# Optimization experiments

Hardware: AMD Instinct MI355X
Metric: run time of the kernel (lower is better)

Reference implementation:

```python
import jax, jax.numpy as jnp
import numpy as np

A = 128       # atom_fea_len
NBR = 41      # nbr_fea_len
H = 128       # h_fea_len_dist == h_fea_len_const
NCONV = 3
EPS = 1e-5    # BatchNorm eps


def leaky(x):
    return jnp.where(x >= 0, x, 0.01 * x)  # LeakyReLU(0.01)


def bn(x2d, g, b):
    # training-mode BatchNorm1d: batch statistics over dim 0 (biased variance)
    mu = x2d.mean(0)
    var = x2d.var(0)
    return g * (x2d - mu) * jax.lax.rsqrt(var + EPS) + b


def setup_inputs() -> dict:
    N, M = 20000, 12
    key = jax.random.key(0)
    ks = jax.random.split(key, 24)
    s = 0.02
    in2 = 2 * A + NBR  # 297
    d = {}
    d["atom_fea"] = jax.random.normal(ks[0], (N, 92), jnp.float32)
    d["nbr_fea"] = jax.random.uniform(ks[1], (N, M, NBR), dtype=jnp.float32)
    d["nbr_fea_offset"] = jax.random.normal(ks[2], (N, M, 3), jnp.float32)
    d["atom_pos"] = jax.random.normal(ks[3], (N, 3), jnp.float32) * 3.0
    d["cells"] = jnp.eye(3, dtype=jnp.float32) * 10.0 + 0.1 * jax.random.normal(ks[4], (3, 3), jnp.float32)
    d["nbr_fea_idx"] = jax.random.randint(ks[5], (N, M), 0, N)
    # embedding
    d["emb_W"] = s * jax.random.normal(ks[6], (A, 92), jnp.float32)
    d["emb_b"] = jnp.zeros((A,), jnp.float32)
    # conv layers (stacked)
    d["convs_W"] = s * jax.random.normal(ks[7], (NCONV, 2 * A, in2), jnp.float32)
    d["convs_b"] = jnp.zeros((NCONV, 2 * A), jnp.float32)
    d["convs_bn1_g"] = jnp.ones((NCONV, 2 * A), jnp.float32)
    d["convs_bn1_b"] = jnp.zeros((NCONV, 2 * A), jnp.float32)
    d["convs_bn2_g"] = jnp.ones((NCONV, A), jnp.float32)
    d["convs_bn2_b"] = jnp.zeros((NCONV, A), jnp.float32)
    # bond_distance head
    d["dist_W"] = s * jax.random.normal(ks[8], (H, in2), jnp.float32)
    d["dist_b"] = jnp.zeros((H,), jnp.float32)
    d["dist_bn_g"] = jnp.ones((H,), jnp.float32)
    d["dist_bn_b"] = jnp.zeros((H,), jnp.float32)
    d["dist2_W"] = s * jax.random.normal(ks[9], (1, H), jnp.float32)
    d["dist2_b"] = jnp.zeros((1,), jnp.float32)
    # bond_constant head
    d["const_W"] = s * jax.random.normal(ks[10], (H, in2), jnp.float32)
    d["const_b"] = jnp.zeros((H,), jnp.float32)
    d["const_bn_g"] = jnp.ones((H,), jnp.float32)
    d["const_bn_b"] = jnp.zeros((H,), jnp.float32)
    d["const2_W"] = s * jax.random.normal(ks[11], (1, H), jnp.float32)
    d["const2_b"] = jnp.zeros((1,), jnp.float32)
    return d


def _forward(atom_fea, nbr_fea, nbr_fea_offset, atom_pos, cells,
             emb_W, emb_b, convs_W, convs_b, convs_bn1_g, convs_bn1_b,
             convs_bn2_g, convs_bn2_b, dist_W, dist_b, dist_bn_g, dist_bn_b,
             dist2_W, dist2_b, const_W, const_b, const_bn_g, const_bn_b,
             const2_W, const2_b, nbr_fea_idx):
    N, M = nbr_fea_idx.shape
    af = atom_fea @ emb_W.T + emb_b  # (N, A) embedding

    # get_distance: PBC distance using fractional offsets and the cell matrix
    nbr_abs = atom_pos[nbr_fea_idx] + jnp.einsum('nmk,kd->nmd', nbr_fea_offset, cells)
    dvec = nbr_abs - atom_pos[:, None, :]
    distance = jnp.sqrt(jnp.sum(dvec * dvec, -1, keepdims=True) + 1e-12)  # (N, M, 1)

    # conv layers: gather -> concat -> linear -> bn -> gate -> sum -> bn -> residual
    for i in range(NCONV):
        total = jnp.concatenate([
            jnp.broadcast_to(af[:, None, :], (N, M, A)),
            af[nbr_fea_idx],
            nbr_fea], axis=2)                                   # (N, M, 2A+NBR)
        g = jnp.einsum('nmf,of->nmo', total, convs_W[i]) + convs_b[i]  # (N, M, 2A)
        g = bn(g.reshape(-1, 2 * A), convs_bn1_g[i], convs_bn1_b[i]).reshape(N, M, 2 * A)
        nbr_filter = jax.nn.sigmoid(g[..., :A])
        nbr_core = leaky(g[..., A:])
        summed = bn((nbr_filter * nbr_core).sum(1), convs_bn2_g[i], convs_bn2_b[i])
        af = leaky(af + summed)

    # bond features
    bond_fea = jnp.concatenate([
        jnp.broadcast_to(af[:, None, :], (N, M, A)),
        af[nbr_fea_idx],
        nbr_fea], axis=2)  # (N, M, 2A+NBR)

    # bond_distance head (LeakyReLU activations)
    bd = jnp.einsum('nmf,hf->nmh', bond_fea, dist_W) + dist_b
    bd = leaky(bn(bd.reshape(-1, H), dist_bn_g, dist_bn_b).reshape(N, M, H))
    bd = leaky(jnp.einsum('nmh,oh->nmo', bd, dist2_W) + dist2_b + distance)  # (N, M, 1)

    # bond_constant head (Softplus activations)
    bc = jnp.einsum('nmf,hf->nmh', bond_fea, const_W) + const_b
    bc = jax.nn.softplus(bn(bc.reshape(-1, H), const_bn_g, const_bn_b).reshape(N, M, H))
    bc = jax.nn.softplus(jnp.einsum('nmh,oh->nmo', bc, const2_W) + const2_b)  # (N, M, 1)

    return jnp.concatenate([bd, bc], axis=-1)  # (N, M, 2)


def reference(atom_fea, nbr_fea, nbr_fea_offset, atom_pos, cells,
              emb_W, emb_b, convs_W, convs_b, convs_bn1_g, convs_bn1_b,
              convs_bn2_g, convs_bn2_b, dist_W, dist_b, dist_bn_g, dist_bn_b,
              dist2_W, dist2_b, const_W, const_b, const_bn_g, const_bn_b,
              const2_W, const2_b, nbr_fea_idx):
    return _forward(atom_fea, nbr_fea, nbr_fea_offset, atom_pos, cells,
                    emb_W, emb_b, convs_W, convs_b, convs_bn1_g, convs_bn1_b,
                    convs_bn2_g, convs_bn2_b, dist_W, dist_b, dist_bn_g, dist_bn_b,
                    dist2_W, dist2_b, const_W, const_b, const_bn_g, const_bn_b,
                    const2_W, const2_b, nbr_fea_idx)
```

## Files before the change

kernel.cpp:

```cpp
#include <hip/hip_runtime.h>
#include <hip/hip_bf16.h>
#include <math.h>

typedef __hip_bfloat16 bf16;

#define AFEA 128
#define NBRF 41
#define IN2 297
#define KP 320
#define TSTR 328
#define TSTRE 104
#define ROWS 64
#define P1 64
#define P2 16
#define WBE_OFF (4 * KP * 256)
#define WBE_SZ (3 * 128 * 32)

typedef __attribute__((ext_vector_type(8))) short bf16x8;
typedef __attribute__((ext_vector_type(4))) float f32x4;

__device__ __forceinline__ unsigned short bfbits(float x) {
    bf16 h = __float2bfloat16(x);
    return *(unsigned short*)&h;
}
__device__ __forceinline__ unsigned int pack2(float x, float y) {
    return (unsigned int)bfbits(x) | ((unsigned int)bfbits(y) << 16);
}
__device__ __forceinline__ float blo(unsigned int u) { return __uint_as_float(u << 16); }
__device__ __forceinline__ float bhi(unsigned int u) { return __uint_as_float(u & 0xffff0000u); }
__device__ __forceinline__ float leakyf(float x) { return x >= 0.f ? x : 0.01f * x; }
__device__ __forceinline__ float sigmoid_fast(float x) {
    return __builtin_amdgcn_rcpf(1.f + __expf(-x));
}
__device__ __forceinline__ float softplus_fast(float x) {
    return fmaxf(x, 0.f) + __logf(1.f + __expf(-fabsf(x)));
}

__device__ __forceinline__ float gpair(unsigned int fu, unsigned int cu,
                                       float aF, float cF, float aC, float cC) {
    float r = sigmoid_fast(fmaf(aF, blo(fu), cF)) * leakyf(fmaf(aC, blo(cu), cC));
    r += sigmoid_fast(fmaf(aF, bhi(fu), cF)) * leakyf(fmaf(aC, bhi(cu), cC));
    return r;
}

__global__ void nbr16_kernel(const float* __restrict__ nbr, unsigned short* __restrict__ nbr16,
                             int NM)
{
    int i = blockIdx.x * blockDim.x + threadIdx.x;
    if (i >= NM * 64) return;
    int k = i & 63, e = i >> 6;
    nbr16[i] = (k < NBRF) ? bfbits(nbr[(size_t)e * NBRF + k]) : 0;
}

__global__ __launch_bounds__(256) void embed_mfma_kernel(
    const float* __restrict__ xf, const unsigned short* __restrict__ WbE,
    const float* __restrict__ b, float* __restrict__ af,
    unsigned short* __restrict__ af16, int N)
{
    __shared__ __align__(16) unsigned short ls[64 * TSTRE];
    int t = threadIdx.x;
    const int e0 = blockIdx.x * 64;
    const int l = t & 63, w = t >> 6, m16 = l & 15, q = l >> 4;

    {
        int r = t >> 2, p = t & 3;
        int n = e0 + r;
        const float* src = xf + (size_t)n * 92;
        unsigned short* dst = ls + r * TSTRE;
        #pragma unroll
        for (int u = 0; u < 6; u++) {
            int k0 = p * 24 + u * 4;
            if (k0 < 92) {
                float4 v = (n < N) ? *(const float4*)(src + k0)
                                   : make_float4(0.f, 0.f, 0.f, 0.f);
                ushort4 h;
                h.x = bfbits(v.x); h.y = bfbits(v.y);
                h.z = bfbits(v.z); h.w = bfbits(v.w);
                *(ushort4*)(dst + k0) = h;
            }
        }
        if (p == 3) {
            ushort4 z = {0, 0, 0, 0};
            *(ushort4*)(dst + 92) = z;
        }
    }

    const unsigned short* bbase = WbE + (size_t)(w * 32 + m16) * 32 + q * 8;
    __syncthreads();

    f32x4 acc[4][2];
    #pragma unroll
    for (int rt = 0; rt < 4; rt++)
        #pragma unroll
        for (int ct = 0; ct < 2; ct++) acc[rt][ct] = (f32x4)0.f;

    const unsigned short* abase = ls + m16 * TSTRE + q * 8;

    #pragma unroll
    for (int kc = 0; kc < 3; kc++) {
        bf16x8 a[4], bfr[2];
        #pragma unroll
        for (int ct = 0; ct < 2; ct++)
            bfr[ct] = *(const bf16x8*)(bbase + kc * 4096 + ct * 512);
        #pragma unroll
        for (int rt = 0; rt < 4; rt++)
            a[rt] = *(const bf16x8*)(abase + rt * 16 * TSTRE + kc * 32);
        #pragma unroll
        for (int rt = 0; rt < 4; rt++)
            #pragma unroll
            for (int ct = 0; ct < 2; ct++)
                acc[rt][ct] = __builtin_amdgcn_mfma_f32_16x16x32_bf16(
                    a[rt], bfr[ct], acc[rt][ct], 0, 0, 0);
    }

    #pragma unroll
    for (int ct = 0; ct < 2; ct++) {
        int col = w * 32 + ct * 16 + m16;
        float bias = b[col];
        #pragma unroll
        for (int rt = 0; rt < 4; rt++) {
            #pragma unroll
            for (int j = 0; j < 4; j++) {
                int n = e0 + rt * 16 + q * 4 + j;
                if (n < N) {
                    float v = acc[rt][ct][j] + bias;
                    af[(size_t)n * AFEA + col] = v;
                    af16[(size_t)n * AFEA + col] = bfbits(v);
                }
            }
        }
    }
}

__global__ void prep_all_kernel(const float* __restrict__ convs_W,
                                const float* __restrict__ dist_W,
                                const float* __restrict__ const_W,
                                const float* __restrict__ emb_W,
                                unsigned short* __restrict__ Wb4,
                                float* __restrict__ zbuf, int nz)
{
    int i = blockIdx.x * blockDim.x + threadIdx.x;
    if (i < nz) zbuf[i] = 0.f;
    if (i >= WBE_OFF + WBE_SZ) return;
    if (i >= WBE_OFF) {
        int r2 = i - WBE_OFF;
        int t32 = r2 & 31, c = (r2 >> 5) & 127, kc = r2 >> 12;
        int k = kc * 32 + t32;
        Wb4[i] = bfbits((k < 92) ? emb_W[(size_t)c * 92 + k] : 0.f);
        return;
    }
    int s = i / (KP * 256);
    int r = i - s * (KP * 256);
    int t32 = r & 31;
    int c = (r >> 5) & 255;
    int kc = r >> 13;
    int k = kc * 32 + t32;
    float v = 0.f;
    if (k < IN2) {
        if (s < 3) v = convs_W[((size_t)s * 256 + c) * IN2 + k];
        else       v = (c < 128) ? dist_W[(size_t)c * IN2 + k]
                                 : const_W[(size_t)(c - 128) * IN2 + k];
    }
    Wb4[i] = bfbits(v);
}

__device__ __forceinline__ void gemm_core(
    const unsigned short* __restrict__ af16, const unsigned short* __restrict__ nbr16,
    const int* __restrict__ idx, const unsigned short* __restrict__ Wb,
    unsigned short* a_tile, int e0, int M, int t, f32x4 (&acc)[4][4])
{
    const int l = t & 63, w = t >> 6;
    const int m16 = l & 15, q = l >> 4;
    const unsigned short* bbase = Wb + (size_t)(w * 64 + m16) * 32 + q * 8;

    {
        int row = t >> 2, p = t & 3;
        int e = e0 + row;
        int n = e / M;
        int j = idx[e];
        const uint4* srcn = (const uint4*)(af16 + (size_t)n * AFEA);
        const uint4* srcj = (const uint4*)(af16 + (size_t)j * AFEA);
        const uint4* srcb = (const uint4*)(nbr16 + (size_t)e * 64);
        uint4* dst = (uint4*)(a_tile + row * TSTR);
        #pragma unroll
        for (int u = 0; u < 4; u++) dst[p + 4 * u] = srcn[p + 4 * u];
        #pragma unroll
        for (int u = 0; u < 4; u++) dst[16 + p + 4 * u] = srcj[p + 4 * u];
        #pragma unroll
        for (int u = 0; u < 2; u++) dst[32 + p + 4 * u] = srcb[p + 4 * u];
    }

    bf16x8 bcur[4], bnxt[4];
    #pragma unroll
    for (int ct = 0; ct < 4; ct++)
        bcur[ct] = *(const bf16x8*)(bbase + ct * 512);
    #pragma unroll
    for (int ct = 0; ct < 4; ct++)
        bnxt[ct] = *(const bf16x8*)(bbase + 8192 + ct * 512);

    __syncthreads();

    #pragma unroll
    for (int rt = 0; rt < 4; rt++)
        #pragma unroll
        for (int ct = 0; ct < 4; ct++) acc[rt][ct] = (f32x4)0.f;

    const unsigned short* abase = a_tile + m16 * TSTR + q * 8;

    #pragma unroll
    for (int kc = 0; kc < KP / 32; kc++) {
        bf16x8 a[4], b2[4];
        if (kc < KP / 32 - 2) {
            #pragma unroll
            for (int ct = 0; ct < 4; ct++)
                b2[ct] = *(const bf16x8*)(bbase + (kc + 2) * 8192 + ct * 512);
        }
        #pragma unroll
        for (int rt = 0; rt < 4; rt++)
            a[rt] = *(const bf16x8*)(abase + rt * 16 * TSTR + kc * 32);
        #pragma unroll
        for (int rt = 0; rt < 4; rt++)
            #pragma unroll
            for (int ct = 0; ct < 4; ct++)
                acc[rt][ct] = __builtin_amdgcn_mfma_f32_16x16x32_bf16(
                    a[rt], bcur[ct], acc[rt][ct], 0, 0, 0);
        if (kc < KP / 32 - 1) {
            #pragma unroll
            for (int ct = 0; ct < 4; ct++) bcur[ct] = bnxt[ct];
        }
        if (kc < KP / 32 - 2) {
            #pragma unroll
            for (int ct = 0; ct < 4; ct++) bnxt[ct] = b2[ct];
        }
    }
}

__global__ __launch_bounds__(256, 3) void gemm_mfma_kernel(
    const unsigned short* __restrict__ af16, const unsigned short* __restrict__ nbr16,
    const int* __restrict__ idx, const unsigned short* __restrict__ Wb,
    const float* __restrict__ bias_a, const float* __restrict__ bias_b,
    unsigned short* __restrict__ g_t, float* __restrict__ part1,
    float* __restrict__ part2, int NM, int M)
{
    __shared__ __align__(16) unsigned short a_tile[ROWS * TSTR];
    int t = threadIdx.x;
    const int e0 = blockIdx.x * ROWS;

    if (blockIdx.x < 16) part2[blockIdx.x * 256 + t] = 0.f;

    f32x4 acc[4][4];
    gemm_core(af16, nbr16, idx, Wb, a_tile, e0, M, t, acc);

    const int l = t & 63, w = t >> 6, m16 = l & 15, q = l >> 4;
    float* pp = part1 + (size_t)(blockIdx.x & (P1 - 1)) * 512;
    #pragma unroll
    for (int ct = 0; ct < 4; ct++) {
        int col = w * 64 + ct * 16 + m16;
        float bias = (col < 128) ? bias_a[col] : bias_b[col - 128];
        float ps = 0.f, pq = 0.f;
        #pragma unroll
        for (int rt = 0; rt < 4; rt++) {
            float v0 = acc[rt][ct][0] + bias;
            float v1 = acc[rt][ct][1] + bias;
            float v2 = acc[rt][ct][2] + bias;
            float v3 = acc[rt][ct][3] + bias;
            ps += (v0 + v1) + (v2 + v3);
            pq += (v0 * v0 + v1 * v1) + (v2 * v2 + v3 * v3);
            uint2 pk;
            pk.x = pack2(v0, v1);
            pk.y = pack2(v2, v3);
            *(uint2*)(g_t + (size_t)col * NM + e0 + rt * 16 + q * 4) = pk;
        }
        ps += __shfl_xor(ps, 16); ps += __shfl_xor(ps, 32);
        pq += __shfl_xor(pq, 16); pq += __shfl_xor(pq, 32);
        if (q == 0) {
            atomicAdd(&pp[col], ps);
            atomicAdd(&pp[256 + col], pq);
        }
    }
}

__global__ __launch_bounds__(256) void gate_kernel(
    const unsigned short* __restrict__ gt, const float* __restrict__ part1,
    const float* __restrict__ gamma, const float* __restrict__ beta,
    float* __restrict__ summed, float* __restrict__ part2,
    float cnt1, int N, int NM)
{
    __shared__ float affA[32], affC[32];
    __shared__ float ls[128 * 17];
    int t = threadIdx.x, w = t >> 6, l = t & 63;
    int ab = blockIdx.x >> 3, pg = blockIdx.x & 7;

    if (t < 32) {
        int ch = (t < 16) ? (pg * 16 + t) : (128 + pg * 16 + (t - 16));
        float s = 0.f, qq = 0.f;
        #pragma unroll 8
        for (int p = 0; p < P1; p++) {
            s += part1[(size_t)p * 512 + ch];
            qq += part1[(size_t)p * 512 + 256 + ch];
        }
        float mean = s / cnt1;
        float var = fmaxf(qq / cnt1 - mean * mean, 0.f);
        float a = gamma[ch] * rsqrtf(var + 1e-5f);
        affA[t] = a;
        affC[t] = beta[ch] - mean * a;
    }
    __syncthreads();

    int n0 = ab * 128 + 2 * l;
    bool a0 = n0 < N, a1 = (n0 + 1) < N;
    float* pp = part2 + (size_t)(blockIdx.x & (P2 - 1)) * 256;

    #pragma unroll
    for (int pi = 0; pi < 4; pi++) {
        int plocal = w * 4 + pi;
        int chf = pg * 16 + plocal;
        float aF = affA[plocal],      cF = affC[plocal];
        float aC = affA[16 + plocal], cC = affC[16 + plocal];
        float s0 = 0.f, s1 = 0.f;
        if (a0) {
            const uint4* F = (const uint4*)(gt + (size_t)chf * NM + (size_t)n0 * 12);
            const uint4* C = (const uint4*)(gt + (size_t)(chf + 128) * NM + (size_t)n0 * 12);
            uint4 f0 = F[0], f1 = F[1], f2 = F[2];
            uint4 c0 = C[0], c1 = C[1], c2 = C[2];
            s0 = gpair(f0.x, c0.x, aF, cF, aC, cC) + gpair(f0.y, c0.y, aF, cF, aC, cC)
               + gpair(f0.z, c0.z, aF, cF, aC, cC) + gpair(f0.w, c0.w, aF, cF, aC, cC)
               + gpair(f1.x, c1.x, aF, cF, aC, cC) + gpair(f1.y, c1.y, aF, cF, aC, cC);
            s1 = gpair(f1.z, c1.z, aF, cF, aC, cC) + gpair(f1.w, c1.w, aF, cF, aC, cC)
               + gpair(f2.x, c2.x, aF, cF, aC, cC) + gpair(f2.y, c2.y, aF, cF, aC, cC)
               + gpair(f2.z, c2.z, aF, cF, aC, cC) + gpair(f2.w, c2.w, aF, cF, aC, cC);
            if (!a1) s1 = 0.f;
            ls[(2 * l) * 17 + plocal] = s0;
            if (a1) ls[(2 * l + 1) * 17 + plocal] = s1;
        }
        float sr = s0 + s1;
        float qr = s0 * s0 + s1 * s1;
        #pragma unroll
        for (int sft = 32; sft > 0; sft >>= 1) {
            sr += __shfl_xor(sr, sft);
            qr += __shfl_xor(qr, sft);
        }
        if (l == 0) {
            atomicAdd(&pp[chf], sr);
            atomicAdd(&pp[128 + chf], qr);
        }
    }
    __syncthreads();

    for (int i = t; i < 128 * 16; i += 256) {
        int a = i >> 4, c = i & 15;
        int n = ab * 128 + a;
        if (n < N) summed[(size_t)n * AFEA + pg * 16 + c] = ls[a * 17 + c];
    }
}

__global__ __launch_bounds__(256) void afup_kernel(
    float* __restrict__ af, unsigned short* __restrict__ af16,
    const float* __restrict__ summed, const float* __restrict__ part2,
    const float* __restrict__ gamma2, const float* __restrict__ beta2,
    float* __restrict__ part1, float cnt2, int total)
{
    __shared__ float a2s[128], c2s[128];
    int t = threadIdx.x;
    if (blockIdx.x < 128) part1[blockIdx.x * 256 + t] = 0.f;
    if (t < 128) {
        float s = 0.f, qq = 0.f;
        #pragma unroll
        for (int p = 0; p < P2; p++) {
            s += part2[(size_t)p * 256 + t];
            qq += part2[(size_t)p * 256 + 128 + t];
        }
        float mean = s / cnt2;
        float var = fmaxf(qq / cnt2 - mean * mean, 0.f);
        float a = gamma2[t] * rsqrtf(var + 1e-5f);
        a2s[t] = a;
        c2s[t] = beta2[t] - mean * a;
    }
    __syncthreads();
    int o = t & 127;
    float a2 = a2s[o], c2 = c2s[o];
    int base = blockIdx.x * 2048 + t;
    #pragma unroll
    for (int k = 0; k < 8; k++) {
        int i = base + k * 256;
        if (i < total) {
            float v = af[i] + a2 * summed[i] + c2;
            v = (v >= 0.f) ? v : 0.01f * v;
            af[i] = v;
            af16[i] = bfbits(v);
        }
    }
}

__global__ __launch_bounds__(256) void head_kernel(
    const unsigned short* __restrict__ gt, const float* __restrict__ part1,
    const float* __restrict__ dbg, const float* __restrict__ cbg,
    const float* __restrict__ dbb, const float* __restrict__ cbb,
    const float* __restrict__ w2d, const float* __restrict__ b2d,
    const float* __restrict__ w2c, const float* __restrict__ b2c,
    const float* __restrict__ pos, const float* __restrict__ off,
    const float* __restrict__ cells, const int* __restrict__ idx,
    float* __restrict__ out, float cnt1, int NM, int M)
{
    __shared__ float a_s[256], c_s[256], w_s[256];
    int t = threadIdx.x;
    {
        float s = 0.f, qq = 0.f;
        #pragma unroll 8
        for (int p = 0; p < P1; p++) {
            s += part1[(size_t)p * 512 + t];
            qq += part1[(size_t)p * 512 + 256 + t];
        }
        float mean = s / cnt1;
        float var = fmaxf(qq / cnt1 - mean * mean, 0.f);
        float g  = (t < 128) ? dbg[t] : cbg[t - 128];
        float be = (t < 128) ? dbb[t] : cbb[t - 128];
        float a = g * rsqrtf(var + 1e-5f);
        a_s[t] = a;
        c_s[t] = be - mean * a;
        w_s[t] = (t < 128) ? w2d[t] : w2c[t - 128];
    }
    __syncthreads();

    int e = blockIdx.x * 512 + t * 2;
    if (e >= NM) return;
    float sd0 = 0.f, sd1 = 0.f, sc0 = 0.f, sc1 = 0.f;
    #pragma unroll 4
    for (int ch = 0; ch < 128; ch++) {
        unsigned int u = *(const unsigned int*)(gt + (size_t)ch * NM + e);
        float a = a_s[ch], c = c_s[ch], wv = w_s[ch];
        sd0 += leakyf(fmaf(a, blo(u), c)) * wv;
        sd1 += leakyf(fmaf(a, bhi(u), c)) * wv;
    }
    #pragma unroll 4
    for (int ch = 128; ch < 256; ch++) {
        unsigned int u = *(const unsigned int*)(gt + (size_t)ch * NM + e);
        float a = a_s[ch], c = c_s[ch], wv = w_s[ch];
        sc0 += softplus_fast(fmaf(a, blo(u), c)) * wv;
        sc1 += softplus_fast(fmaf(a, bhi(u), c)) * wv;
    }
    float dist[2];
    #pragma unroll
    for (int h = 0; h < 2; h++) {
        int eb = e + h;
        int n = eb / M;
        int j = idx[eb];
        float o0 = off[(size_t)eb * 3 + 0];
        float o1 = off[(size_t)eb * 3 + 1];
        float o2 = off[(size_t)eb * 3 + 2];
        float d0 = o0 * cells[0] + o1 * cells[3] + o2 * cells[6] + pos[(size_t)j * 3 + 0] - pos[(size_t)n * 3 + 0];
        float d1 = o0 * cells[1] + o1 * cells[4] + o2 * cells[7] + pos[(size_t)j * 3 + 1] - pos[(size_t)n * 3 + 1];
        float d2 = o0 * cells[2] + o1 * cells[5] + o2 * cells[8] + pos[(size_t)j * 3 + 2] - pos[(size_t)n * 3 + 2];
        dist[h] = sqrtf(d0 * d0 + d1 * d1 + d2 * d2 + 1e-12f);
    }
    float bd = b2d[0], bc = b2c[0];
    float4 o4;
    o4.x = leakyf(sd0 + bd + dist[0]);
    o4.y = softplus_fast(sc0 + bc);
    o4.z = leakyf(sd1 + bd + dist[1]);
    o4.w = softplus_fast(sc1 + bc);
    *(float4*)(out + (size_t)e * 2) = o4;
}

extern "C" void kernel_launch(void* const* d_in, const int* in_sizes, int n_in,
                              void* d_out, int out_size, void* d_ws, size_t ws_size,
                              hipStream_t stream) {
    const float* atom_fea   = (const float*)d_in[0];
    const float* nbr_fea    = (const float*)d_in[1];
    const float* nbr_off    = (const float*)d_in[2];
    const float* atom_pos   = (const float*)d_in[3];
    const float* cells      = (const float*)d_in[4];
    const int*   idx        = (const int*)d_in[5];
    const float* emb_W      = (const float*)d_in[6];
    const float* emb_b      = (const float*)d_in[7];
    const float* convs_W    = (const float*)d_in[8];
    const float* convs_b    = (const float*)d_in[9];
    const float* bn1g       = (const float*)d_in[10];
    const float* bn1b       = (const float*)d_in[11];
    const float* bn2g       = (const float*)d_in[12];
    const float* bn2b       = (const float*)d_in[13];
    const float* dist_W     = (const float*)d_in[14];
    const float* dist_b     = (const float*)d_in[15];
    const float* dist_bn_g  = (const float*)d_in[16];
    const float* dist_bn_b  = (const float*)d_in[17];
    const float* dist2_W    = (const float*)d_in[18];
    const float* dist2_b    = (const float*)d_in[19];
    const float* const_W    = (const float*)d_in[20];
    const float* const_b    = (const float*)d_in[21];
    const float* const_bn_g = (const float*)d_in[22];
    const float* const_bn_b = (const float*)d_in[23];
    const float* const2_W   = (const float*)d_in[24];
    const float* const2_b   = (const float*)d_in[25];

    const int N  = in_sizes[0] / 92;
    const int M  = in_sizes[5] / N;
    const int NM = N * M;

    char* ws = (char*)d_ws;
    size_t off = 0;
    float* af             = (float*)(ws + off); off += (size_t)N * AFEA * 4;
    float* summed         = (float*)(ws + off); off += (size_t)N * AFEA * 4;
    unsigned short* af16  = (unsigned short*)(ws + off); off += (size_t)N * AFEA * 2;
    unsigned short* Wb4   = (unsigned short*)(ws + off); off += (size_t)(WBE_OFF + WBE_SZ) * 2;
    float* part1          = (float*)(ws + off); off += (size_t)P1 * 512 * 4;
    float* part2          = (float*)(ws + off); off += (size_t)P2 * 256 * 4;
    unsigned short* g_t   = (unsigned short*)(ws + off); off += (size_t)NM * 256 * 2;
    unsigned short* nbr16 = (unsigned short*)(ws + off); off += (size_t)NM * 64 * 2;

    const int NPART = P1 * 512 + P2 * 256;

    prep_all_kernel<<<(WBE_OFF + WBE_SZ + 255) / 256, 256, 0, stream>>>(
        convs_W, dist_W, const_W, emb_W, Wb4, part1, NPART);
    nbr16_kernel<<<(NM * 64 + 255) / 256, 256, 0, stream>>>(nbr_fea, nbr16, NM);
    embed_mfma_kernel<<<(N + 63) / 64, 256, 0, stream>>>(
        atom_fea, Wb4 + WBE_OFF, emb_b, af, af16, N);

    const int gblocks = NM / ROWS;
    const int gateblocks = ((N + 127) / 128) * 8;

    for (int i = 0; i < 3; i++) {
        const unsigned short* Wbi = Wb4 + (size_t)i * KP * 256;
        const float* cb = convs_b + (size_t)i * 256;
        gemm_mfma_kernel<<<gblocks, 256, 0, stream>>>(
            af16, nbr16, idx, Wbi, cb, cb + 128, g_t, part1, part2, NM, M);
        gate_kernel<<<gateblocks, 256, 0, stream>>>(
            g_t, part1, bn1g + (size_t)i * 256, bn1b + (size_t)i * 256,
            summed, part2, (float)NM, N, NM);
        afup_kernel<<<(N * AFEA + 2047) / 2048, 256, 0, stream>>>(
            af, af16, summed, part2, bn2g + (size_t)i * 128, bn2b + (size_t)i * 128,
            part1, (float)N, N * AFEA);
    }

    {
        gemm_mfma_kernel<<<gblocks, 256, 0, stream>>>(
            af16, nbr16, idx, Wb4 + (size_t)3 * KP * 256, dist_b, const_b,
            g_t, part1, part2, NM, M);
        head_kernel<<<(NM + 511) / 512, 256, 0, stream>>>(
            g_t, part1, dist_bn_g, const_bn_g, dist_bn_b, const_bn_b,
            dist2_W, dist2_b, const2_W, const2_b,
            atom_pos, nbr_off, cells, idx, (float*)d_out, (float)NM, NM, M);
    }
}
```

Measured before the change: 605.1 us.

## Process two row tiles per GEMM block, prefetching the second tile's gathers

```diff
diff --git a/kernel.cpp b/kernel.cpp
--- a/kernel.cpp
+++ b/kernel.cpp
@@ -164,32 +164,10 @@
     Wb4[i] = bfbits(v);
 }
 
-__device__ __forceinline__ void gemm_core(
-    const unsigned short* __restrict__ af16, const unsigned short* __restrict__ nbr16,
-    const int* __restrict__ idx, const unsigned short* __restrict__ Wb,
-    unsigned short* a_tile, int e0, int M, int t, f32x4 (&acc)[4][4])
-{
-    const int l = t & 63, w = t >> 6;
-    const int m16 = l & 15, q = l >> 4;
-    const unsigned short* bbase = Wb + (size_t)(w * 64 + m16) * 32 + q * 8;
-
-    {
-        int row = t >> 2, p = t & 3;
-        int e = e0 + row;
-        int n = e / M;
-        int j = idx[e];
-        const uint4* srcn = (const uint4*)(af16 + (size_t)n * AFEA);
-        const uint4* srcj = (const uint4*)(af16 + (size_t)j * AFEA);
-        const uint4* srcb = (const uint4*)(nbr16 + (size_t)e * 64);
-        uint4* dst = (uint4*)(a_tile + row * TSTR);
-        #pragma unroll
-        for (int u = 0; u < 4; u++) dst[p + 4 * u] = srcn[p + 4 * u];
-        #pragma unroll
-        for (int u = 0; u < 4; u++) dst[16 + p + 4 * u] = srcj[p + 4 * u];
-        #pragma unroll
-        for (int u = 0; u < 2; u++) dst[32 + p + 4 * u] = srcb[p + 4 * u];
-    }
-
+__device__ __forceinline__ void mfma_tile(
+    const unsigned short* __restrict__ abase,
+    const unsigned short* __restrict__ bbase, f32x4 (&acc)[4][4])
+{
     bf16x8 bcur[4], bnxt[4];
     #pragma unroll
     for (int ct = 0; ct < 4; ct++)
@@ -204,8 +182,6 @@
     for (int rt = 0; rt < 4; rt++)
         #pragma unroll
         for (int ct = 0; ct < 4; ct++) acc[rt][ct] = (f32x4)0.f;
-
-    const unsigned short* abase = a_tile + m16 * TSTR + q * 8;
 
     #pragma unroll
     for (int kc = 0; kc < KP / 32; kc++) {
@@ -235,24 +211,11 @@
     }
 }
 
-__global__ __launch_bounds__(256, 3) void gemm_mfma_kernel(
-    const unsigned short* __restrict__ af16, const unsigned short* __restrict__ nbr16,
-    const int* __restrict__ idx, const unsigned short* __restrict__ Wb,
+__device__ __forceinline__ void gemm_epilogue(
+    f32x4 (&acc)[4][4], int e0, int w, int m16, int q,
     const float* __restrict__ bias_a, const float* __restrict__ bias_b,
-    unsigned short* __restrict__ g_t, float* __restrict__ part1,
-    float* __restrict__ part2, int NM, int M)
-{
-    __shared__ __align__(16) unsigned short a_tile[ROWS * TSTR];
-    int t = threadIdx.x;
-    const int e0 = blockIdx.x * ROWS;
-
-    if (blockIdx.x < 16) part2[blockIdx.x * 256 + t] = 0.f;
-
-    f32x4 acc[4][4];
-    gemm_core(af16, nbr16, idx, Wb, a_tile, e0, M, t, acc);
-
-    const int l = t & 63, w = t >> 6, m16 = l & 15, q = l >> 4;
-    float* pp = part1 + (size_t)(blockIdx.x & (P1 - 1)) * 512;
+    unsigned short* __restrict__ g_t, float* __restrict__ pp, int NM)
+{
     #pragma unroll
     for (int ct = 0; ct < 4; ct++) {
         int col = w * 64 + ct * 16 + m16;
@@ -277,6 +240,87 @@
             atomicAdd(&pp[col], ps);
             atomicAdd(&pp[256 + col], pq);
         }
+    }
+}
+
+__global__ __launch_bounds__(256, 3) void gemm_mfma_kernel(
+    const unsigned short* __restrict__ af16, const unsigned short* __restrict__ nbr16,
+    const int* __restrict__ idx, const unsigned short* __restrict__ Wb,
+    const float* __restrict__ bias_a, const float* __restrict__ bias_b,
+    unsigned short* __restrict__ g_t, float* __restrict__ part1,
+    float* __restrict__ part2, int NM, int M, int ntiles)
+{
+    __shared__ __align__(16) unsigned short a_tile[ROWS * TSTR];
+    const int t = threadIdx.x;
+    const int l = t & 63, w = t >> 6, m16 = l & 15, q = l >> 4;
+    const unsigned short* bbase = Wb + (size_t)(w * 64 + m16) * 32 + q * 8;
+    const unsigned short* abase = a_tile + m16 * TSTR + q * 8;
+
+    if (blockIdx.x < 16) part2[blockIdx.x * 256 + t] = 0.f;
+
+    const int t0 = blockIdx.x * 2;
+    const int t1 = t0 + 1;
+    const bool has1 = (t1 < ntiles);
+    const int e0 = t0 * ROWS;
+
+    const int row = t >> 2, p = t & 3;
+    const int er0 = e0 + row;
+    const int er1 = has1 ? (t1 * ROWS + row) : er0;
+
+    int ja = idx[er0];
+    int jb = idx[er1];
+    int na = er0 / M;
+    int nb = er1 / M;
+
+    const uint4* srcn0 = (const uint4*)(af16 + (size_t)na * AFEA);
+    const uint4* srcj0 = (const uint4*)(af16 + (size_t)ja * AFEA);
+    const uint4* srcb0 = (const uint4*)(nbr16 + (size_t)er0 * 64);
+    uint4 a0[4], j0[4], b0[2];
+    #pragma unroll
+    for (int u = 0; u < 4; u++) a0[u] = srcn0[p + 4 * u];
+    #pragma unroll
+    for (int u = 0; u < 4; u++) j0[u] = srcj0[p + 4 * u];
+    #pragma unroll
+    for (int u = 0; u < 2; u++) b0[u] = srcb0[p + 4 * u];
+
+    const uint4* srcj1 = (const uint4*)(af16 + (size_t)jb * AFEA);
+    const uint4* srcb1 = (const uint4*)(nbr16 + (size_t)er1 * 64);
+    uint4 j1[4], b1[2];
+    #pragma unroll
+    for (int u = 0; u < 4; u++) j1[u] = srcj1[p + 4 * u];
+    #pragma unroll
+    for (int u = 0; u < 2; u++) b1[u] = srcb1[p + 4 * u];
+
+    uint4* dst = (uint4*)(a_tile + row * TSTR);
+    #pragma unroll
+    for (int u = 0; u < 4; u++) dst[p + 4 * u] = a0[u];
+    #pragma unroll
+    for (int u = 0; u < 4; u++) dst[16 + p + 4 * u] = j0[u];
+    #pragma unroll
+    for (int u = 0; u < 2; u++) dst[32 + p + 4 * u] = b0[u];
+
+    float* pp = part1 + (size_t)(blockIdx.x & (P1 - 1)) * 512;
+
+    f32x4 acc[4][4];
+    mfma_tile(abase, bbase, acc);
+    gemm_epilogue(acc, e0, w, m16, q, bias_a, bias_b, g_t, pp, NM);
+
+    if (has1) {
+        __syncthreads();
+
+        const uint4* srcn1 = (const uint4*)(af16 + (size_t)nb * AFEA);
+        uint4 a1[4];
+        #pragma unroll
+        for (int u = 0; u < 4; u++) a1[u] = srcn1[p + 4 * u];
+        #pragma unroll
+        for (int u = 0; u < 4; u++) dst[16 + p + 4 * u] = j1[u];
+        #pragma unroll
+        for (int u = 0; u < 2; u++) dst[32 + p + 4 * u] = b1[u];
+        #pragma unroll
+        for (int u = 0; u < 4; u++) dst[p + 4 * u] = a1[u];
+
+        mfma_tile(abase, bbase, acc);
+        gemm_epilogue(acc, t1 * ROWS, w, m16, q, bias_a, bias_b, g_t, pp, NM);
     }
 }
 
@@ -333,8 +377,9 @@
             ls[(2 * l) * 17 + plocal] = s0;
             if (a1) ls[(2 * l + 1) * 17 + plocal] = s1;
         }
+        float q0 = s0 * s0, q1 = s1 * s1;
         float sr = s0 + s1;
-        float qr = s0 * s0 + s1 * s1;
+        float qr = q0 + q1;
         #pragma unroll
         for (int sft = 32; sft > 0; sft >>= 1) {
             sr += __shfl_xor(sr, sft);
@@ -516,13 +561,14 @@
         atom_fea, Wb4 + WBE_OFF, emb_b, af, af16, N);
 
     const int gblocks = NM / ROWS;
+    const int ggrid = (gblocks + 1) / 2;
     const int gateblocks = ((N + 127) / 128) * 8;
 
     for (int i = 0; i < 3; i++) {
         const unsigned short* Wbi = Wb4 + (size_t)i * KP * 256;
         const float* cb = convs_b + (size_t)i * 256;
-        gemm_mfma_kernel<<<gblocks, 256, 0, stream>>>(
-            af16, nbr16, idx, Wbi, cb, cb + 128, g_t, part1, part2, NM, M);
+        gemm_mfma_kernel<<<ggrid, 256, 0, stream>>>(
+            af16, nbr16, idx, Wbi, cb, cb + 128, g_t, part1, part2, NM, M, gblocks);
         gate_kernel<<<gateblocks, 256, 0, stream>>>(
             g_t, part1, bn1g + (size_t)i * 256, bn1b + (size_t)i * 256,
             summed, part2, (float)NM, N, NM);
@@ -532,9 +578,9 @@
     }
 
     {
-        gemm_mfma_kernel<<<gblocks, 256, 0, stream>>>(
+        gemm_mfma_kernel<<<ggrid, 256, 0, stream>>>(
             af16, nbr16, idx, Wb4 + (size_t)3 * KP * 256, dist_b, const_b,
-            g_t, part1, part2, NM, M);
+            g_t, part1, part2, NM, M, gblocks);
         head_kernel<<<(NM + 511) / 512, 256, 0, stream>>>(
             g_t, part1, dist_bn_g, const_bn_g, dist_bn_b, const_bn_b,
             dist2_W, dist2_b, const2_W, const2_b,
```

After: 703.1 us. 16.2% more time.
